# Optimization experiments

Hardware: AMD Instinct MI355X
Metric: run time of the kernel (lower is better)

## Reference

```python
import jax, jax.numpy as jnp
import numpy as np

_KX = jnp.array([[1., 0., -1.], [2., 0., -2.], [1., 0., -1.]], dtype=jnp.float32).reshape(1, 1, 3, 3)
_KY = jnp.transpose(_KX, (0, 1, 3, 2))  # ky = kx.transpose(2,3)


def _sobel(x, k):
    # x: [B,1,H,W], k: [1,1,3,3]; SAME padding=1, stride 1
    return jax.lax.conv_general_dilated(
        x, k, window_strides=(1, 1), padding=((1, 1), (1, 1)),
        dimension_numbers=('NCHW', 'OIHW', 'NCHW'))


def setup_inputs() -> dict:
    key = jax.random.key(0)
    k1, k2 = jax.random.split(key)
    sr = jax.random.normal(k1, (32, 1, 1024, 1024), dtype=jnp.float32)
    hr = jax.random.normal(k2, (32, 1, 1024, 1024), dtype=jnp.float32)
    return {"sr": sr, "hr": hr}


def reference(sr, hr):
    gx_sr = _sobel(sr, _KX)
    gy_sr = _sobel(sr, _KY)
    gx_hr = _sobel(hr, _KX)
    gy_hr = _sobel(hr, _KY)
    return jnp.mean(jnp.abs(gx_sr - gx_hr) + jnp.abs(gy_sr - gy_hr))
```

## Files before the change

### kernel.cpp

```cpp
#include <hip/hip_runtime.h>


#define IMG_H 1024
#define IMG_W 1024
#define IMG_B 32
#define CHUNK_H 32
#define NCHUNK (IMG_H / CHUNK_H)

__device__ __forceinline__ void load_row(const float* __restrict__ sr,
                                         const float* __restrict__ hr,
                                         size_t img_off, int x0, int yin,
                                         float4& s, float4& t) {
    float dl = 0.f, dr = 0.f;
    float4 d = make_float4(0.f, 0.f, 0.f, 0.f);
    if ((unsigned)yin < (unsigned)IMG_H) {
        size_t row = img_off + (size_t)yin * IMG_W;
        const float4 a = *reinterpret_cast<const float4*>(sr + row + x0);
        const float4 b = *reinterpret_cast<const float4*>(hr + row + x0);
        d.x = a.x - b.x; d.y = a.y - b.y; d.z = a.z - b.z; d.w = a.w - b.w;
        if (x0 > 0)           dl = sr[row + x0 - 1] - hr[row + x0 - 1];
        if (x0 + 4 < IMG_W)   dr = sr[row + x0 + 4] - hr[row + x0 + 4];
    }
    s.x = dl  + 2.f * d.x + d.y;
    s.y = d.x + 2.f * d.y + d.z;
    s.z = d.y + 2.f * d.z + d.w;
    s.w = d.z + 2.f * d.w + dr;
    t.x = dl  - d.y;
    t.y = d.x - d.z;
    t.z = d.y - d.w;
    t.w = d.z - dr;
}

__global__ __launch_bounds__(256) void edge_loss_kernel(
        const float* __restrict__ sr, const float* __restrict__ hr,
        float* __restrict__ out, float invN) {
    const int chunk = blockIdx.x;
    const int b     = blockIdx.y;
    const int tid   = threadIdx.x;
    const int x0    = tid * 4;
    const size_t img_off = (size_t)b * IMG_H * IMG_W;
    const int y0 = chunk * CHUNK_H;

    float4 s0, s1, s2, t0, t1, t2;
    load_row(sr, hr, img_off, x0, y0 - 1, s0, t0);
    load_row(sr, hr, img_off, x0, y0,     s1, t1);

    float acc = 0.f;
    #pragma unroll 4
    for (int y = y0; y < y0 + CHUNK_H; ++y) {
        load_row(sr, hr, img_off, x0, y + 1, s2, t2);
        float gx, gy;
        gx = t0.x + 2.f * t1.x + t2.x;  gy = s0.x - s2.x;  acc += fabsf(gx) + fabsf(gy);
        gx = t0.y + 2.f * t1.y + t2.y;  gy = s0.y - s2.y;  acc += fabsf(gx) + fabsf(gy);
        gx = t0.z + 2.f * t1.z + t2.z;  gy = s0.z - s2.z;  acc += fabsf(gx) + fabsf(gy);
        gx = t0.w + 2.f * t1.w + t2.w;  gy = s0.w - s2.w;  acc += fabsf(gx) + fabsf(gy);
        s0 = s1; t0 = t1; s1 = s2; t1 = t2;
    }

    #pragma unroll
    for (int off = 32; off > 0; off >>= 1)
        acc += __shfl_down(acc, off, 64);

    __shared__ float wsum[4];
    const int wave = tid >> 6, lane = tid & 63;
    if (lane == 0) wsum[wave] = acc;
    __syncthreads();
    if (tid == 0) {
        float bsum = wsum[0] + wsum[1] + wsum[2] + wsum[3];
        atomicAdd(out, bsum * invN);
    }
}

extern "C" void kernel_launch(void* const* d_in, const int* in_sizes, int n_in,
                              void* d_out, int out_size, void* d_ws, size_t ws_size,
                              hipStream_t stream) {
    const float* sr = (const float*)d_in[0];
    const float* hr = (const float*)d_in[1];
    float* out = (float*)d_out;

    hipMemsetAsync(out, 0, sizeof(float), stream);

    dim3 grid(NCHUNK, IMG_B);
    const float invN = 1.0f / (float)((size_t)IMG_B * IMG_H * IMG_W);
    edge_loss_kernel<<<grid, 256, 0, stream>>>(sr, hr, out, invN);
}
```

Measured before the change: 284.7 us.

## Share row halos via wave shuffles and prefetch rows two ahead

Left and right halo values now come from neighbouring lanes through shuffles, so only lanes at the edges of each wave issue scalar halo loads. Raw row loads are software-pipelined two rows ahead so memory latency overlaps with compute. The loop is fully unrolled, and the chunk height is halved to double the number of blocks. Row clamping plus a multiplier mask replaces the branch on out-of-range rows. The costs are more registers and more per-block halo rows, which add redundant traffic.

Measured after the change: 283.0 us. Within noise of the previous version (-0.6%).

```diff
diff --git a/kernel.cpp b/kernel.cpp
--- a/kernel.cpp
+++ b/kernel.cpp
@@ -4,23 +4,44 @@
 #define IMG_H 1024
 #define IMG_W 1024
 #define IMG_B 32
-#define CHUNK_H 32
+#define CHUNK_H 16
 #define NCHUNK (IMG_H / CHUNK_H)
 
-__device__ __forceinline__ void load_row(const float* __restrict__ sr,
-                                         const float* __restrict__ hr,
-                                         size_t img_off, int x0, int yin,
-                                         float4& s, float4& t) {
-    float dl = 0.f, dr = 0.f;
-    float4 d = make_float4(0.f, 0.f, 0.f, 0.f);
-    if ((unsigned)yin < (unsigned)IMG_H) {
-        size_t row = img_off + (size_t)yin * IMG_W;
-        const float4 a = *reinterpret_cast<const float4*>(sr + row + x0);
-        const float4 b = *reinterpret_cast<const float4*>(hr + row + x0);
-        d.x = a.x - b.x; d.y = a.y - b.y; d.z = a.z - b.z; d.w = a.w - b.w;
-        if (x0 > 0)           dl = sr[row + x0 - 1] - hr[row + x0 - 1];
-        if (x0 + 4 < IMG_W)   dr = sr[row + x0 + 4] - hr[row + x0 + 4];
-    }
+struct Raw { float4 a, b; float aL, bL, aR, bR; };
+
+__device__ __forceinline__ Raw load_raw(const float* __restrict__ sr,
+                                        const float* __restrict__ hr,
+                                        size_t img, int yin, int x0, int lane) {
+    const int yc = min(max(yin, 0), IMG_H - 1);
+    const size_t row = img + (size_t)yc * IMG_W;
+    Raw r;
+    r.a = *reinterpret_cast<const float4*>(sr + row + x0);
+    r.b = *reinterpret_cast<const float4*>(hr + row + x0);
+    r.aL = 0.f; r.bL = 0.f; r.aR = 0.f; r.bR = 0.f;
+    if (lane == 0 && x0 > 0)          { r.aL = sr[row + x0 - 1]; r.bL = hr[row + x0 - 1]; }
+    if (lane == 63 && x0 + 4 < IMG_W) { r.aR = sr[row + x0 + 4]; r.bR = hr[row + x0 + 4]; }
+    return r;
+}
+
+__device__ __forceinline__ Raw zero_raw() {
+    Raw r;
+    r.a = make_float4(0.f, 0.f, 0.f, 0.f);
+    r.b = make_float4(0.f, 0.f, 0.f, 0.f);
+    r.aL = r.bL = r.aR = r.bR = 0.f;
+    return r;
+}
+
+__device__ __forceinline__ void process(const Raw& r, float m, int lane,
+                                        float4& s, float4& t) {
+    float4 d;
+    d.x = (r.a.x - r.b.x) * m;
+    d.y = (r.a.y - r.b.y) * m;
+    d.z = (r.a.z - r.b.z) * m;
+    d.w = (r.a.w - r.b.w) * m;
+    float dl = __shfl_up(d.w, 1, 64);
+    float dr = __shfl_down(d.x, 1, 64);
+    if (lane == 0)  dl = (r.aL - r.bL) * m;
+    if (lane == 63) dr = (r.aR - r.bR) * m;
     s.x = dl  + 2.f * d.x + d.y;
     s.y = d.x + 2.f * d.y + d.z;
     s.z = d.y + 2.f * d.z + d.w;
@@ -37,24 +58,36 @@
     const int chunk = blockIdx.x;
     const int b     = blockIdx.y;
     const int tid   = threadIdx.x;
+    const int lane  = tid & 63;
     const int x0    = tid * 4;
-    const size_t img_off = (size_t)b * IMG_H * IMG_W;
+    const size_t img = (size_t)b * IMG_H * IMG_W;
     const int y0 = chunk * CHUNK_H;
 
-    float4 s0, s1, s2, t0, t1, t2;
-    load_row(sr, hr, img_off, x0, y0 - 1, s0, t0);
-    load_row(sr, hr, img_off, x0, y0,     s1, t1);
+    Raw rm = load_raw(sr, hr, img, y0 - 1, x0, lane);
+    Raw r0 = load_raw(sr, hr, img, y0,     x0, lane);
+    Raw rA = load_raw(sr, hr, img, y0 + 1, x0, lane);
+    Raw rB = load_raw(sr, hr, img, y0 + 2, x0, lane);
+
+    float4 s0, t0, s1, t1, s2, t2;
+    process(rm, (y0 > 0) ? 1.f : 0.f, lane, s0, t0);
+    process(r0, 1.f, lane, s1, t1);
 
     float acc = 0.f;
-    #pragma unroll 4
+    #pragma unroll
     for (int y = y0; y < y0 + CHUNK_H; ++y) {
-        load_row(sr, hr, img_off, x0, y + 1, s2, t2);
+        Raw rn = (y + 3 <= y0 + CHUNK_H)
+                     ? load_raw(sr, hr, img, y + 3, x0, lane)
+                     : zero_raw();
+        process(rA, (y + 1 < IMG_H) ? 1.f : 0.f, lane, s2, t2);
+
         float gx, gy;
         gx = t0.x + 2.f * t1.x + t2.x;  gy = s0.x - s2.x;  acc += fabsf(gx) + fabsf(gy);
         gx = t0.y + 2.f * t1.y + t2.y;  gy = s0.y - s2.y;  acc += fabsf(gx) + fabsf(gy);
         gx = t0.z + 2.f * t1.z + t2.z;  gy = s0.z - s2.z;  acc += fabsf(gx) + fabsf(gy);
         gx = t0.w + 2.f * t1.w + t2.w;  gy = s0.w - s2.w;  acc += fabsf(gx) + fabsf(gy);
+
         s0 = s1; t0 = t1; s1 = s2; t1 = t2;
+        rA = rB; rB = rn;
     }
 
     #pragma unroll
@@ -62,7 +95,7 @@
         acc += __shfl_down(acc, off, 64);
 
     __shared__ float wsum[4];
-    const int wave = tid >> 6, lane = tid & 63;
+    const int wave = tid >> 6;
     if (lane == 0) wsum[wave] = acc;
     __syncthreads();
     if (tid == 0) {
```

## Batch row loads into registers and share horizontal halos via wave shuffles

Applied to the files above, without the earlier changes.

Each block now handles 8 rows instead of 32, loading all 10 input rows (with clamped indices) up front into register arrays so the loads are issued together rather than serially inside the loop. Horizontal neighbour values come from wave cross-lane shuffles instead of per-thread scalar global loads, and only the edge lanes fetch halo pixels. Out-of-image rows and columns are zeroed with multiplicative masks instead of branches. The cost is more redundant halo rows (10 loaded per 8 computed), four times more blocks and atomics, and higher register pressure.

Measured after the change: 275.7 us. -3.1%, faster.

```diff
diff --git a/kernel.cpp b/kernel.cpp
--- a/kernel.cpp
+++ b/kernel.cpp
@@ -4,23 +4,23 @@
 #define IMG_H 1024
 #define IMG_W 1024
 #define IMG_B 32
-#define CHUNK_H 32
-#define NCHUNK (IMG_H / CHUNK_H)
+#define CH 8
+#define NROW (CH + 2)
+#define NCHUNK (IMG_H / CH)
 
-__device__ __forceinline__ void load_row(const float* __restrict__ sr,
-                                         const float* __restrict__ hr,
-                                         size_t img_off, int x0, int yin,
-                                         float4& s, float4& t) {
-    float dl = 0.f, dr = 0.f;
-    float4 d = make_float4(0.f, 0.f, 0.f, 0.f);
-    if ((unsigned)yin < (unsigned)IMG_H) {
-        size_t row = img_off + (size_t)yin * IMG_W;
-        const float4 a = *reinterpret_cast<const float4*>(sr + row + x0);
-        const float4 b = *reinterpret_cast<const float4*>(hr + row + x0);
-        d.x = a.x - b.x; d.y = a.y - b.y; d.z = a.z - b.z; d.w = a.w - b.w;
-        if (x0 > 0)           dl = sr[row + x0 - 1] - hr[row + x0 - 1];
-        if (x0 + 4 < IMG_W)   dr = sr[row + x0 + 4] - hr[row + x0 + 4];
-    }
+__device__ __forceinline__ void row_st(const float4& a, const float4& b,
+                                       float ha, float hb, float m, float hm,
+                                       int lane, float4& s, float4& t) {
+    float4 d;
+    d.x = (a.x - b.x) * m;
+    d.y = (a.y - b.y) * m;
+    d.z = (a.z - b.z) * m;
+    d.w = (a.w - b.w) * m;
+    const float dh = (ha - hb) * (m * hm);
+    float dl = __shfl_up(d.w, 1, 64);
+    float dr = __shfl_down(d.x, 1, 64);
+    if (lane == 0)  dl = dh;
+    if (lane == 63) dr = dh;
     s.x = dl  + 2.f * d.x + d.y;
     s.y = d.x + 2.f * d.y + d.z;
     s.z = d.y + 2.f * d.z + d.w;
@@ -37,23 +37,58 @@
     const int chunk = blockIdx.x;
     const int b     = blockIdx.y;
     const int tid   = threadIdx.x;
+    const int lane  = tid & 63;
     const int x0    = tid * 4;
-    const size_t img_off = (size_t)b * IMG_H * IMG_W;
-    const int y0 = chunk * CHUNK_H;
+    const size_t img = (size_t)b * IMG_H * IMG_W;
+    const int y0 = chunk * CH;
 
-    float4 s0, s1, s2, t0, t1, t2;
-    load_row(sr, hr, img_off, x0, y0 - 1, s0, t0);
-    load_row(sr, hr, img_off, x0, y0,     s1, t1);
+    const bool isL = (lane == 0);
+    const bool isR = (lane == 63);
+    const int  hx  = isL ? x0 - 1 : x0 + 4;
+    const float hm = (isL ? (x0 > 0) : (x0 + 4 < IMG_W)) ? 1.f : 0.f;
+    const int  hxc = min(max(hx, 0), IMG_W - 1);
+
+    float4 A[NROW], B[NROW];
+    float  hA[NROW], hB[NROW];
+    #pragma unroll
+    for (int i = 0; i < NROW; ++i) { hA[i] = 0.f; hB[i] = 0.f; }
+
+    #pragma unroll
+    for (int i = 0; i < NROW; ++i) {
+        const int yc = min(max(y0 - 1 + i, 0), IMG_H - 1);
+        const size_t row = img + (size_t)yc * IMG_W;
+        A[i] = *reinterpret_cast<const float4*>(sr + row + x0);
+        B[i] = *reinterpret_cast<const float4*>(hr + row + x0);
+    }
+    if (isL || isR) {
+        #pragma unroll
+        for (int i = 0; i < NROW; ++i) {
+            const int yc = min(max(y0 - 1 + i, 0), IMG_H - 1);
+            const size_t row = img + (size_t)yc * IMG_W;
+            hA[i] = sr[row + hxc];
+            hB[i] = hr[row + hxc];
+        }
+    }
+
+    const float mtop = (y0 > 0) ? 1.f : 0.f;
+    const float mbot = (y0 + CH < IMG_H) ? 1.f : 0.f;
+
+    float4 s0, t0, s1, t1, s2, t2;
+    row_st(A[0], B[0], hA[0], hB[0], mtop, hm, lane, s0, t0);
+    row_st(A[1], B[1], hA[1], hB[1], 1.f,  hm, lane, s1, t1);
 
     float acc = 0.f;
-    #pragma unroll 4
-    for (int y = y0; y < y0 + CHUNK_H; ++y) {
-        load_row(sr, hr, img_off, x0, y + 1, s2, t2);
+    #pragma unroll
+    for (int i = 2; i < NROW; ++i) {
+        const float m = (i == NROW - 1) ? mbot : 1.f;
+        row_st(A[i], B[i], hA[i], hB[i], m, hm, lane, s2, t2);
+
         float gx, gy;
         gx = t0.x + 2.f * t1.x + t2.x;  gy = s0.x - s2.x;  acc += fabsf(gx) + fabsf(gy);
         gx = t0.y + 2.f * t1.y + t2.y;  gy = s0.y - s2.y;  acc += fabsf(gx) + fabsf(gy);
         gx = t0.z + 2.f * t1.z + t2.z;  gy = s0.z - s2.z;  acc += fabsf(gx) + fabsf(gy);
         gx = t0.w + 2.f * t1.w + t2.w;  gy = s0.w - s2.w;  acc += fabsf(gx) + fabsf(gy);
+
         s0 = s1; t0 = t1; s1 = s2; t1 = t2;
     }
 
@@ -62,11 +97,11 @@
         acc += __shfl_down(acc, off, 64);
 
     __shared__ float wsum[4];
-    const int wave = tid >> 6, lane = tid & 63;
+    const int wave = tid >> 6;
     if (lane == 0) wsum[wave] = acc;
     __syncthreads();
     if (tid == 0) {
-        float bsum = wsum[0] + wsum[1] + wsum[2] + wsum[3];
+        const float bsum = wsum[0] + wsum[1] + wsum[2] + wsum[3];
         atomicAdd(out, bsum * invN);
     }
 }
```

## Stage row tiles in LDS via direct global-to-LDS loads with shuffle halos

Applied to the files above, without the earlier changes.

Each block now handles 8 output rows and first copies its 10 input rows of both images into LDS with the direct global-to-LDS load builtin, then computes the Sobel difference from LDS. Horizontal neighbours come from wave shuffles instead of extra scalar global loads. Boundary rows are clamped and zeroed with a mask. This removes the redundant unaligned halo loads, but smaller chunks raise the halo-row overhead (10 rows read per 8 output rows) and 80KB of LDS per block limits occupancy.

Measured after the change: 278.3 us. 2.2% less time.

```diff
diff --git a/kernel.cpp b/kernel.cpp
--- a/kernel.cpp
+++ b/kernel.cpp
@@ -4,23 +4,28 @@
 #define IMG_H 1024
 #define IMG_W 1024
 #define IMG_B 32
-#define CHUNK_H 32
-#define NCHUNK (IMG_H / CHUNK_H)
+#define CH 8
+#define NROW (CH + 2)
+#define NCHUNK (IMG_H / CH)
 
-__device__ __forceinline__ void load_row(const float* __restrict__ sr,
-                                         const float* __restrict__ hr,
-                                         size_t img_off, int x0, int yin,
-                                         float4& s, float4& t) {
-    float dl = 0.f, dr = 0.f;
-    float4 d = make_float4(0.f, 0.f, 0.f, 0.f);
-    if ((unsigned)yin < (unsigned)IMG_H) {
-        size_t row = img_off + (size_t)yin * IMG_W;
-        const float4 a = *reinterpret_cast<const float4*>(sr + row + x0);
-        const float4 b = *reinterpret_cast<const float4*>(hr + row + x0);
-        d.x = a.x - b.x; d.y = a.y - b.y; d.z = a.z - b.z; d.w = a.w - b.w;
-        if (x0 > 0)           dl = sr[row + x0 - 1] - hr[row + x0 - 1];
-        if (x0 + 4 < IMG_W)   dr = sr[row + x0 + 4] - hr[row + x0 + 4];
-    }
+typedef __attribute__((address_space(1))) const void GCV;
+typedef __attribute__((address_space(3))) void LDSV;
+
+__device__ __forceinline__ void row_st_lds(const float* __restrict__ A,
+                                           const float* __restrict__ Bb,
+                                           int x0, float m, int lane,
+                                           float4& s, float4& t) {
+    const float4 a  = *reinterpret_cast<const float4*>(A + x0);
+    const float4 bb = *reinterpret_cast<const float4*>(Bb + x0);
+    float4 d;
+    d.x = (a.x - bb.x) * m;
+    d.y = (a.y - bb.y) * m;
+    d.z = (a.z - bb.z) * m;
+    d.w = (a.w - bb.w) * m;
+    float dl = __shfl_up(d.w, 1, 64);
+    float dr = __shfl_down(d.x, 1, 64);
+    if (lane == 0)  dl = (x0 > 0)           ? (A[x0 - 1] - Bb[x0 - 1]) * m : 0.f;
+    if (lane == 63) dr = (x0 + 4 < IMG_W)   ? (A[x0 + 4] - Bb[x0 + 4]) * m : 0.f;
     s.x = dl  + 2.f * d.x + d.y;
     s.y = d.x + 2.f * d.y + d.z;
     s.z = d.y + 2.f * d.z + d.w;
@@ -34,26 +39,54 @@
 __global__ __launch_bounds__(256) void edge_loss_kernel(
         const float* __restrict__ sr, const float* __restrict__ hr,
         float* __restrict__ out, float invN) {
+    __shared__ float lds[2 * NROW * IMG_W];
+
     const int chunk = blockIdx.x;
     const int b     = blockIdx.y;
     const int tid   = threadIdx.x;
-    const int x0    = tid * 4;
-    const size_t img_off = (size_t)b * IMG_H * IMG_W;
-    const int y0 = chunk * CHUNK_H;
+    const int wave  = tid >> 6;
+    const int lane  = tid & 63;
+    const size_t img = (size_t)b * IMG_H * IMG_W;
+    const int y0 = chunk * CH;
 
-    float4 s0, s1, s2, t0, t1, t2;
-    load_row(sr, hr, img_off, x0, y0 - 1, s0, t0);
-    load_row(sr, hr, img_off, x0, y0,     s1, t1);
+    {
+        const int inp   = wave >> 1;
+        const float* src = inp ? hr : sr;
+        #pragma unroll
+        for (int j = 0; j < 20; ++j) {
+            const int rem = (wave & 1) * 20 + j;
+            const int r   = rem >> 2;
+            const int q   = rem & 3;
+            const int yc  = min(max(y0 - 1 + r, 0), IMG_H - 1);
+            const float* g = src + img + (size_t)yc * IMG_W + q * 256 + lane * 4;
+            float* l = &lds[(inp * 40 + rem) * 256];
+            __builtin_amdgcn_global_load_lds((GCV*)g, (LDSV*)l, 16, 0, 0);
+        }
+    }
+    __syncthreads();
+
+    const int x0 = tid * 4;
+    const float* Ab = lds;
+    const float* Bb = lds + NROW * IMG_W;
+    const float mtop = (y0 > 0) ? 1.f : 0.f;
+    const float mbot = (y0 + CH < IMG_H) ? 1.f : 0.f;
+
+    float4 s0, t0, s1, t1, s2, t2;
+    row_st_lds(Ab,          Bb,          x0, mtop, lane, s0, t0);
+    row_st_lds(Ab + IMG_W,  Bb + IMG_W,  x0, 1.f,  lane, s1, t1);
 
     float acc = 0.f;
-    #pragma unroll 4
-    for (int y = y0; y < y0 + CHUNK_H; ++y) {
-        load_row(sr, hr, img_off, x0, y + 1, s2, t2);
+    #pragma unroll
+    for (int r = 2; r < NROW; ++r) {
+        const float m = (r == NROW - 1) ? mbot : 1.f;
+        row_st_lds(Ab + r * IMG_W, Bb + r * IMG_W, x0, m, lane, s2, t2);
+
         float gx, gy;
         gx = t0.x + 2.f * t1.x + t2.x;  gy = s0.x - s2.x;  acc += fabsf(gx) + fabsf(gy);
         gx = t0.y + 2.f * t1.y + t2.y;  gy = s0.y - s2.y;  acc += fabsf(gx) + fabsf(gy);
         gx = t0.z + 2.f * t1.z + t2.z;  gy = s0.z - s2.z;  acc += fabsf(gx) + fabsf(gy);
         gx = t0.w + 2.f * t1.w + t2.w;  gy = s0.w - s2.w;  acc += fabsf(gx) + fabsf(gy);
+
         s0 = s1; t0 = t1; s1 = s2; t1 = t2;
     }
 
@@ -61,14 +94,11 @@
     for (int off = 32; off > 0; off >>= 1)
         acc += __shfl_down(acc, off, 64);
 
-    __shared__ float wsum[4];
-    const int wave = tid >> 6, lane = tid & 63;
-    if (lane == 0) wsum[wave] = acc;
     __syncthreads();
-    if (tid == 0) {
-        float bsum = wsum[0] + wsum[1] + wsum[2] + wsum[3];
-        atomicAdd(out, bsum * invN);
-    }
+    if (lane == 0) lds[wave] = acc;
+    __syncthreads();
+    if (tid == 0)
+        atomicAdd(out, (lds[0] + lds[1] + lds[2] + lds[3]) * invN);
 }
 
 extern "C" void kernel_launch(void* const* d_in, const int* in_sizes, int n_in,
```
